# Kernel tuning notes

Hardware: AMD Instinct MI355X
Metric: run time of the kernel (lower is better)

The kernel has to match this reference:

```python
import jax, jax.numpy as jnp
import numpy as np

N_NODES = 50000
N_EDGES = 800000
NODE_DIM = 64
EDGE_DIM = 32
HID = 128


def _lin_init(key, fan_in, fan_out):
    # torch nn.Linear default: U(-1/sqrt(fan_in), 1/sqrt(fan_in))
    bound = 1.0 / np.sqrt(fan_in)
    kw, kb = jax.random.split(key)
    W = jax.random.uniform(kw, (fan_in, fan_out), jnp.float32, -bound, bound)
    b = jax.random.uniform(kb, (fan_out,), jnp.float32, -bound, bound)
    return W, b


def setup_inputs() -> dict:
    key = jax.random.key(0)
    ks = jax.random.split(key, 10)
    h = jax.random.normal(ks[0], (N_NODES, NODE_DIM), dtype=jnp.float32)
    x = jax.random.normal(ks[1], (N_NODES, 3), dtype=jnp.float32) * 10.0
    edge_idx = jax.random.randint(ks[2], (2, N_EDGES), 0, N_NODES)
    edge_dist = jax.random.uniform(ks[3], (N_EDGES,), jnp.float32) * 15.0
    m_in_dim = 2 * NODE_DIM + EDGE_DIM
    W_e1, b_e1 = _lin_init(ks[4], 1, EDGE_DIM)
    W_e2, b_e2 = _lin_init(ks[5], EDGE_DIM, EDGE_DIM)
    W_n1, b_n1 = _lin_init(ks[6], m_in_dim, HID)
    W_n2, b_n2 = _lin_init(ks[7], HID, NODE_DIM)
    W_c1, b_c1 = _lin_init(ks[8], m_in_dim, HID)
    W_c2, _ = _lin_init(ks[9], HID, 1)  # coord_mlp final layer has bias=False
    return dict(h=h, x=x, edge_dist=edge_dist,
                W_e1=W_e1, b_e1=b_e1, W_e2=W_e2, b_e2=b_e2,
                W_n1=W_n1, b_n1=b_n1, W_n2=W_n2, b_n2=b_n2,
                W_c1=W_c1, b_c1=b_c1, W_c2=W_c2,
                edge_idx=edge_idx)


def reference(h, x, edge_dist, W_e1, b_e1, W_e2, b_e2, W_n1, b_n1,
              W_n2, b_n2, W_c1, b_c1, W_c2, edge_idx):
    src, dst = edge_idx[0], edge_idx[1]
    n = h.shape[0]
    # edge_mlp: Linear(1,edge_dim) -> SiLU -> Linear(edge_dim,edge_dim)
    edge_attr = jax.nn.silu(edge_dist[:, None] @ W_e1 + b_e1) @ W_e2 + b_e2  # [E, edge_dim]
    m_in = jnp.concatenate([h[src], h[dst], edge_attr], axis=-1)  # [E, 2*node+edge]
    # node_mlp: Linear -> SiLU -> Linear
    m = jax.nn.silu(m_in @ W_n1 + b_n1) @ W_n2 + b_n2  # [E, node_dim]
    h_agg = jax.ops.segment_sum(m, dst, num_segments=n)
    # coord_mlp: Linear -> SiLU -> Linear(,1,bias=False)
    coord_w = jax.nn.silu(m_in @ W_c1 + b_c1) @ W_c2  # [E, 1]
    dir_vec = x[src] - x[dst]  # [E, 3]
    dir_len = jnp.maximum(jnp.linalg.norm(dir_vec, axis=-1, keepdims=True), 1e-8)
    x_agg = jax.ops.segment_sum(coord_w * (dir_vec / dir_len), dst, num_segments=n)
    return (h + h_agg, x + x_agg)
```

## Files before the change

kernel.cpp:

```cpp
#include <hip/hip_runtime.h>
#include <cstdint>
#include <cstddef>

#define E_CNT 800000
#define N_CNT 50000
#define NT 6250

typedef short bf16x8 __attribute__((ext_vector_type(8)));
typedef short s16x4 __attribute__((ext_vector_type(4)));
typedef float f32x4 __attribute__((ext_vector_type(4)));
typedef uint32_t u32x4 __attribute__((ext_vector_type(4)));

#define OFF_CURSOR 0
#define OFF_WFN 200064
#define OFF_WFC 241024
#define OFF_W2F 281984
#define OFF_BIASN 298368
#define OFF_BIASC 298880
#define OFF_SRC 299520
#define OFF_DST 3499520
#define OFF_DIST 6699520
#define OFF_HB 8299520
#define REQ_FULL 14699520

__device__ __forceinline__ short f2bf(float v) {
  uint32_t u = __builtin_bit_cast(uint32_t, v);
  u = (u + 0x7FFFu + ((u >> 16) & 1u)) >> 16;
  return (short)u;
}
__device__ __forceinline__ float bf2f(short s) {
  uint32_t u = ((uint32_t)(uint16_t)s) << 16;
  return __builtin_bit_cast(float, u);
}
__device__ __forceinline__ uint32_t pack2(float lo, float hi) {
  return ((uint32_t)(uint16_t)f2bf(hi) << 16) | (uint32_t)(uint16_t)f2bf(lo);
}
__device__ __forceinline__ uint32_t cvtpk(float lo, float hi) {
  uint32_t r;
  asm("v_cvt_pk_bf16_f32 %0, %1, %2" : "=v"(r) : "v"(lo), "v"(hi));
  return r;
}
__device__ __forceinline__ float silu_f(float v) {
  return v * (1.0f / (1.0f + __expf(-v)));
}

template <bool FULL>
__global__ void k_pre(const float* __restrict__ h, const float* __restrict__ x,
                      float* __restrict__ out, short* __restrict__ hb,
                      const int* __restrict__ eidx, int* __restrict__ cursor,
                      const float* __restrict__ W1n, const float* __restrict__ W1c,
                      const float* __restrict__ We2, const float* __restrict__ bn1,
                      const float* __restrict__ bc1, const float* __restrict__ be2,
                      const float* __restrict__ Wn2,
                      short* __restrict__ Wfn, short* __restrict__ Wfc,
                      short* __restrict__ W2f, float* __restrict__ biasn,
                      float* __restrict__ biasc) {
  const int b = (int)blockIdx.x;
  if (b < 3272) {
    const int i = b * 256 + (int)threadIdx.x;
    if (i < 800000) {
      const f32x4 v = ((const f32x4*)h)[i];
      ((f32x4*)out)[i] = v;
      if (FULL) {
        s16x4 p;
#pragma unroll
        for (int j = 0; j < 4; ++j) p[j] = f2bf(v[j]);
        *(s16x4*)(hb + i * 4) = p;
      }
    } else if (i < 837500) {
      ((f32x4*)out)[i] = ((const f32x4*)x)[i - 800000];
    }
  } else if (b < 3297) {
    const int idx = (b - 3272) * 4 + ((int)threadIdx.x >> 6);
    const int l = (int)threadIdx.x & 63;
    if (idx < 80) {
      const int fid = (idx < 40) ? idx : (idx - 40);
      const float* W1 = (idx < 40) ? W1n : W1c;
      short* Wf = (idx < 40) ? Wfn : Wfc;
      const int kt = fid >> 3, nt = fid & 7;
      const int feat = (l & 15) * 8 + nt;
      const int k0 = kt * 32 + (l >> 4) * 8;
      bf16x8 v;
#pragma unroll
      for (int j = 0; j < 8; ++j) {
        const int k = k0 + j;
        float val;
        if (k < 128) {
          val = W1[k * 128 + feat];
        } else {
          float s = 0.f;
          for (int cc = 0; cc < 32; ++cc)
            s = fmaf(We2[(k - 128) * 32 + cc], W1[(128 + cc) * 128 + feat], s);
          val = s;
        }
        v[j] = f2bf(val);
      }
      *(bf16x8*)&Wf[(fid * 64 + l) * 8] = v;
    } else if (idx < 96) {
      const int fid = idx - 80;
      const int kt2 = fid >> 2, nt2 = fid & 3;
      bf16x8 v;
#pragma unroll
      for (int j = 0; j < 8; ++j)
        v[j] = f2bf(Wn2[(kt2 * 32 + (l >> 4) * 8 + j) * 64 + nt2 * 16 + (l & 15)]);
      *(bf16x8*)&W2f[(fid * 64 + l) * 8] = v;
    } else if (idx == 96) {
      for (int col = l; col < 128; col += 64) {
        float sn = bn1[col], sc = bc1[col];
        for (int cc = 0; cc < 32; ++cc) {
          sn = fmaf(be2[cc], W1n[(128 + cc) * 128 + col], sn);
          sc = fmaf(be2[cc], W1c[(128 + cc) * 128 + col], sc);
        }
        biasn[col] = sn;
        biasc[col] = sc;
      }
    }
  } else if (FULL) {
    const int e = (b - 3297) * 256 + (int)threadIdx.x;
    if (e < E_CNT) atomicAdd(&cursor[eidx[E_CNT + e]], 1);
  }
}

__global__ __launch_bounds__(1024) void k_scan(int* __restrict__ cursor) {
  __shared__ int part[1024];
  const int t = (int)threadIdx.x;
  const int b0 = t * 49;
  int n = N_CNT - b0;
  n = n < 0 ? 0 : (n > 49 ? 49 : n);
  int s = 0;
  for (int i = 0; i < n; ++i) s += cursor[b0 + i];
  part[t] = s;
  __syncthreads();
  for (int off = 1; off < 1024; off <<= 1) {
    const int u = (t >= off) ? part[t - off] : 0;
    __syncthreads();
    part[t] += u;
    __syncthreads();
  }
  int run = (t == 0) ? 0 : part[t - 1];
  for (int i = 0; i < n; ++i) {
    const int old = cursor[b0 + i];
    cursor[b0 + i] = run;
    run += old;
  }
}

__global__ void k_fill(const int* __restrict__ eidx, const float* __restrict__ edist,
                       int* __restrict__ cursor, int* __restrict__ src_s,
                       int* __restrict__ dst_s, short* __restrict__ dist_s) {
  const int e = (int)(blockIdx.x * 256 + threadIdx.x);
  if (e < E_CNT) {
    const int d = eidx[E_CNT + e];
    const int pos = atomicAdd(&cursor[d], 1);
    src_s[pos] = eidx[e];
    dst_s[pos] = d;
    dist_s[pos] = f2bf(edist[e]);
  }
}

template <bool SORTED>
__global__ __launch_bounds__(256, 2) void k_main(
    const float* __restrict__ h, const short* __restrict__ hb,
    const float* __restrict__ x, const float* __restrict__ edist,
    const float* __restrict__ We1, const float* __restrict__ be1,
    const float* __restrict__ bn2, const float* __restrict__ Wc2,
    const int* __restrict__ eidx,
    const int* __restrict__ src_s, const int* __restrict__ dst_s,
    const short* __restrict__ dist_s,
    const short* __restrict__ Wfn, const short* __restrict__ Wfc,
    const short* __restrict__ W2f,
    const float* __restrict__ biasn, const float* __restrict__ biasc,
    float* __restrict__ out, float* __restrict__ xo) {
  __shared__ __align__(16) short scr[4][16 * 136];

  const int tid = (int)threadIdx.x;
  const int w = tid >> 6, l = tid & 63, g = l >> 4, c = l & 15;
  const f32x4 vzero = {0.f, 0.f, 0.f, 0.f};
  const int half = (int)(gridDim.x >> 1);

  if ((int)blockIdx.x < half) {
    short* myscr = &scr[w][0];

    float we1s[8], be1s[8];
#pragma unroll
    for (int j = 0; j < 8; ++j) { we1s[j] = We1[g * 8 + j]; be1s[j] = be1[g * 8 + j]; }
    float bias1[8];
#pragma unroll
    for (int nt = 0; nt < 8; ++nt) bias1[nt] = biasn[c * 8 + nt];
    float bias2[4];
#pragma unroll
    for (int nt = 0; nt < 4; ++nt) bias2[nt] = bn2[nt * 16 + c];

    int t = (int)blockIdx.x;
    int ps0 = 0, ps1 = 0, pd0 = 0, pd1 = 0;
    float pdd0 = 0.f, pdd1 = 0.f;
    if (t < NT) {
      const int e0 = t * 128 + w * 32 + 2 * c, e1 = e0 + 1;
      if (SORTED) {
        ps0 = src_s[e0]; ps1 = src_s[e1];
        pd0 = dst_s[e0]; pd1 = dst_s[e1];
        pdd0 = bf2f(dist_s[e0]); pdd1 = bf2f(dist_s[e1]);
      } else {
        ps0 = eidx[e0]; ps1 = eidx[e1];
        pd0 = eidx[E_CNT + e0]; pd1 = eidx[E_CNT + e1];
        pdd0 = edist[e0]; pdd1 = edist[e1];
      }
    }

    for (; t < NT; t += half) {
      const short* wft = Wfn;
      const short* w2t = W2f;
      asm volatile("" : "+v"(wft), "+v"(w2t));

      const int s0 = ps0, s1 = ps1, d0 = pd0, d1 = pd1;
      const float dd0 = pdd0, dd1 = pdd1;

      const int tn = t + half;
      if (tn < NT) {
        const int e0 = tn * 128 + w * 32 + 2 * c, e1 = e0 + 1;
        if (SORTED) {
          ps0 = src_s[e0]; ps1 = src_s[e1];
          pd0 = dst_s[e0]; pd1 = dst_s[e1];
          pdd0 = bf2f(dist_s[e0]); pdd1 = bf2f(dist_s[e1]);
        } else {
          ps0 = eidx[e0]; ps1 = eidx[e1];
          pd0 = eidx[E_CNT + e0]; pd1 = eidx[E_CNT + e1];
          pdd0 = edist[e0]; pdd1 = edist[e1];
        }
      }

      f32x4 acc[2][8];
#pragma unroll
      for (int mt = 0; mt < 2; ++mt)
#pragma unroll
        for (int nt = 0; nt < 8; ++nt) acc[mt][nt] = vzero;

#pragma unroll
      for (int kt = 0; kt < 5; ++kt) {
        bf16x8 a0, a1;
        if (kt < 4) {
          const size_t r0 = (size_t)((kt < 2) ? s0 : d0) * 64 + (kt & 1) * 32 + g * 8;
          const size_t r1 = (size_t)((kt < 2) ? s1 : d1) * 64 + (kt & 1) * 32 + g * 8;
          if (SORTED) {
            a0 = *(const bf16x8*)&hb[r0];
            a1 = *(const bf16x8*)&hb[r1];
          } else {
            const f32x4 pa = *(const f32x4*)(h + r0), pb = *(const f32x4*)(h + r0 + 4);
            const f32x4 qa = *(const f32x4*)(h + r1), qb = *(const f32x4*)(h + r1 + 4);
            u32x4 u0 = {pack2(pa[0], pa[1]), pack2(pa[2], pa[3]),
                        pack2(pb[0], pb[1]), pack2(pb[2], pb[3])};
            u32x4 u1 = {pack2(qa[0], qa[1]), pack2(qa[2], qa[3]),
                        pack2(qb[0], qb[1]), pack2(qb[2], qb[3])};
            a0 = __builtin_bit_cast(bf16x8, u0);
            a1 = __builtin_bit_cast(bf16x8, u1);
          }
        } else {
          float t0[8], t1[8];
#pragma unroll
          for (int j = 0; j < 8; ++j) {
            t0[j] = silu_f(fmaf(dd0, we1s[j], be1s[j]));
            t1[j] = silu_f(fmaf(dd1, we1s[j], be1s[j]));
          }
          u32x4 u0 = {cvtpk(t0[0], t0[1]), cvtpk(t0[2], t0[3]),
                      cvtpk(t0[4], t0[5]), cvtpk(t0[6], t0[7])};
          u32x4 u1 = {cvtpk(t1[0], t1[1]), cvtpk(t1[2], t1[3]),
                      cvtpk(t1[4], t1[5]), cvtpk(t1[6], t1[7])};
          a0 = __builtin_bit_cast(bf16x8, u0);
          a1 = __builtin_bit_cast(bf16x8, u1);
        }
#pragma unroll
        for (int nt = 0; nt < 8; ++nt) {
          const bf16x8 b = *(const bf16x8*)&wft[(((kt << 3) + nt) << 9) + (l << 3)];
          acc[0][nt] = __builtin_amdgcn_mfma_f32_16x16x32_bf16(a0, b, acc[0][nt], 0, 0, 0);
          acc[1][nt] = __builtin_amdgcn_mfma_f32_16x16x32_bf16(a1, b, acc[1][nt], 0, 0, 0);
        }
      }

      f32x4 acc2[2][4];
#pragma unroll
      for (int nt = 0; nt < 4; ++nt) { acc2[0][nt] = vzero; acc2[1][nt] = vzero; }

#pragma unroll
      for (int mt = 0; mt < 2; ++mt) {
#pragma unroll
        for (int r = 0; r < 4; ++r) {
          const float v0 = silu_f(acc[mt][0][r] + bias1[0]);
          const float v1 = silu_f(acc[mt][1][r] + bias1[1]);
          const float v2 = silu_f(acc[mt][2][r] + bias1[2]);
          const float v3 = silu_f(acc[mt][3][r] + bias1[3]);
          const float v4 = silu_f(acc[mt][4][r] + bias1[4]);
          const float v5 = silu_f(acc[mt][5][r] + bias1[5]);
          const float v6 = silu_f(acc[mt][6][r] + bias1[6]);
          const float v7 = silu_f(acc[mt][7][r] + bias1[7]);
          u32x4 pkv = {cvtpk(v0, v1), cvtpk(v2, v3), cvtpk(v4, v5), cvtpk(v6, v7)};
          *(u32x4*)&myscr[(4 * g + r) * 136 + c * 8] = pkv;
        }
#pragma unroll
        for (int kt2 = 0; kt2 < 4; ++kt2) {
          const bf16x8 a2 = *(const bf16x8*)&myscr[c * 136 + kt2 * 32 + g * 8];
#pragma unroll
          for (int nt2 = 0; nt2 < 4; ++nt2) {
            const bf16x8 b2 = *(const bf16x8*)&w2t[(((kt2 << 2) + nt2) << 9) + (l << 3)];
            acc2[mt][nt2] = __builtin_amdgcn_mfma_f32_16x16x32_bf16(a2, b2, acc2[mt][nt2], 0, 0, 0);
          }
        }
      }

      int des[8];
#pragma unroll
      for (int s = 0; s < 8; ++s)
        des[s] = __shfl((s & 1) ? d1 : d0, 4 * g + (s >> 1));

      float run[4];
      int cur = des[0];
#pragma unroll
      for (int nt2 = 0; nt2 < 4; ++nt2) run[nt2] = acc2[0][nt2][0] + bias2[nt2];
#pragma unroll
      for (int s = 1; s < 8; ++s) {
        const int mt = s & 1, r = s >> 1;
        if (des[s] == cur) {
#pragma unroll
          for (int nt2 = 0; nt2 < 4; ++nt2) run[nt2] += acc2[mt][nt2][r] + bias2[nt2];
        } else {
#pragma unroll
          for (int nt2 = 0; nt2 < 4; ++nt2)
            unsafeAtomicAdd(&out[(size_t)cur * 64 + nt2 * 16 + c], run[nt2]);
          cur = des[s];
#pragma unroll
          for (int nt2 = 0; nt2 < 4; ++nt2) run[nt2] = acc2[mt][nt2][r] + bias2[nt2];
        }
      }
#pragma unroll
      for (int nt2 = 0; nt2 < 4; ++nt2)
        unsafeAtomicAdd(&out[(size_t)cur * 64 + nt2 * 16 + c], run[nt2]);
    }
  } else {
    float we1s[8], be1s[8];
#pragma unroll
    for (int j = 0; j < 8; ++j) { we1s[j] = We1[g * 8 + j]; be1s[j] = be1[g * 8 + j]; }
    float b1c[8], wc2l[8];
#pragma unroll
    for (int nt = 0; nt < 8; ++nt) {
      b1c[nt] = biasc[c * 8 + nt];
      wc2l[nt] = Wc2[c * 8 + nt];
    }

    int t = (int)blockIdx.x - half;
    int ps0 = 0, ps1 = 0, pd0 = 0, pd1 = 0;
    float pdd0 = 0.f, pdd1 = 0.f;
    if (t < NT) {
      const int e0 = t * 128 + w * 32 + 2 * c, e1 = e0 + 1;
      if (SORTED) {
        ps0 = src_s[e0]; ps1 = src_s[e1];
        pd0 = dst_s[e0]; pd1 = dst_s[e1];
        pdd0 = bf2f(dist_s[e0]); pdd1 = bf2f(dist_s[e1]);
      } else {
        ps0 = eidx[e0]; ps1 = eidx[e1];
        pd0 = eidx[E_CNT + e0]; pd1 = eidx[E_CNT + e1];
        pdd0 = edist[e0]; pdd1 = edist[e1];
      }
    }

    for (; t < NT; t += half) {
      const short* wft = Wfc;
      asm volatile("" : "+v"(wft));

      const int s0 = ps0, s1 = ps1, d0 = pd0, d1 = pd1;
      const float dd0 = pdd0, dd1 = pdd1;

      const int tn = t + half;
      if (tn < NT) {
        const int e0 = tn * 128 + w * 32 + 2 * c, e1 = e0 + 1;
        if (SORTED) {
          ps0 = src_s[e0]; ps1 = src_s[e1];
          pd0 = dst_s[e0]; pd1 = dst_s[e1];
          pdd0 = bf2f(dist_s[e0]); pdd1 = bf2f(dist_s[e1]);
        } else {
          ps0 = eidx[e0]; ps1 = eidx[e1];
          pd0 = eidx[E_CNT + e0]; pd1 = eidx[E_CNT + e1];
          pdd0 = edist[e0]; pdd1 = edist[e1];
        }
      }

      f32x4 acc[2][8];
#pragma unroll
      for (int mt = 0; mt < 2; ++mt)
#pragma unroll
        for (int nt = 0; nt < 8; ++nt) acc[mt][nt] = vzero;

#pragma unroll
      for (int kt = 0; kt < 5; ++kt) {
        bf16x8 a0, a1;
        if (kt < 4) {
          const size_t r0 = (size_t)((kt < 2) ? s0 : d0) * 64 + (kt & 1) * 32 + g * 8;
          const size_t r1 = (size_t)((kt < 2) ? s1 : d1) * 64 + (kt & 1) * 32 + g * 8;
          if (SORTED) {
            a0 = *(const bf16x8*)&hb[r0];
            a1 = *(const bf16x8*)&hb[r1];
          } else {
            const f32x4 pa = *(const f32x4*)(h + r0), pb = *(const f32x4*)(h + r0 + 4);
            const f32x4 qa = *(const f32x4*)(h + r1), qb = *(const f32x4*)(h + r1 + 4);
            u32x4 u0 = {pack2(pa[0], pa[1]), pack2(pa[2], pa[3]),
                        pack2(pb[0], pb[1]), pack2(pb[2], pb[3])};
            u32x4 u1 = {pack2(qa[0], qa[1]), pack2(qa[2], qa[3]),
                        pack2(qb[0], qb[1]), pack2(qb[2], qb[3])};
            a0 = __builtin_bit_cast(bf16x8, u0);
            a1 = __builtin_bit_cast(bf16x8, u1);
          }
        } else {
          float t0[8], t1[8];
#pragma unroll
          for (int j = 0; j < 8; ++j) {
            t0[j] = silu_f(fmaf(dd0, we1s[j], be1s[j]));
            t1[j] = silu_f(fmaf(dd1, we1s[j], be1s[j]));
          }
          u32x4 u0 = {cvtpk(t0[0], t0[1]), cvtpk(t0[2], t0[3]),
                      cvtpk(t0[4], t0[5]), cvtpk(t0[6], t0[7])};
          u32x4 u1 = {cvtpk(t1[0], t1[1]), cvtpk(t1[2], t1[3]),
                      cvtpk(t1[4], t1[5]), cvtpk(t1[6], t1[7])};
          a0 = __builtin_bit_cast(bf16x8, u0);
          a1 = __builtin_bit_cast(bf16x8, u1);
        }
#pragma unroll
        for (int nt = 0; nt < 8; ++nt) {
          const bf16x8 b = *(const bf16x8*)&wft[(((kt << 3) + nt) << 9) + (l << 3)];
          acc[0][nt] = __builtin_amdgcn_mfma_f32_16x16x32_bf16(a0, b, acc[0][nt], 0, 0, 0);
          acc[1][nt] = __builtin_amdgcn_mfma_f32_16x16x32_bf16(a1, b, acc[1][nt], 0, 0, 0);
        }
      }

      float p0[4], p1[4];
#pragma unroll
      for (int r = 0; r < 4; ++r) {
        float a = 0.f, bsum = 0.f;
#pragma unroll
        for (int nt = 0; nt < 8; ++nt) {
          a += silu_f(acc[0][nt][r] + b1c[nt]) * wc2l[nt];
          bsum += silu_f(acc[1][nt][r] + b1c[nt]) * wc2l[nt];
        }
        p0[r] = a; p1[r] = bsum;
      }
#pragma unroll
      for (int m = 1; m < 16; m <<= 1)
#pragma unroll
        for (int r = 0; r < 4; ++r) {
          p0[r] += __shfl_xor(p0[r], m);
          p1[r] += __shfl_xor(p1[r], m);
        }

      const int mt = c & 1, rr = c >> 1;
      const int dA = __shfl(d0, 4 * g + rr), dB = __shfl(d1, 4 * g + rr);
      const int sA = __shfl(s0, 4 * g + rr), sB = __shfl(s1, 4 * g + rr);
      const int dstE = mt ? dB : dA;
      const int srcE = mt ? sB : sA;
      if (c < 8) {
        const float cwp0 = (rr == 0) ? p0[0] : (rr == 1) ? p0[1] : (rr == 2) ? p0[2] : p0[3];
        const float cwp1 = (rr == 0) ? p1[0] : (rr == 1) ? p1[1] : (rr == 2) ? p1[2] : p1[3];
        const float cw = mt ? cwp1 : cwp0;
        const float ax = x[srcE * 3 + 0] - x[dstE * 3 + 0];
        const float ay = x[srcE * 3 + 1] - x[dstE * 3 + 1];
        const float az = x[srcE * 3 + 2] - x[dstE * 3 + 2];
        float len = sqrtf(fmaf(ax, ax, fmaf(ay, ay, az * az)));
        len = fmaxf(len, 1e-8f);
        const float scl = cw / len;
        float vx = scl * ax, vy = scl * ay, vz = scl * az;
#pragma unroll
        for (int k = 1; k < 8; k <<= 1) {
          const float tx = __shfl(vx, l - k);
          const float ty = __shfl(vy, l - k);
          const float tz = __shfl(vz, l - k);
          const int td = __shfl(dstE, l - k);
          if (c >= k && td == dstE) { vx += tx; vy += ty; vz += tz; }
        }
        const int dnx = __shfl(dstE, l + 1);
        if (c == 7 || dnx != dstE) {
          unsafeAtomicAdd(&xo[dstE * 3 + 0], vx);
          unsafeAtomicAdd(&xo[dstE * 3 + 1], vy);
          unsafeAtomicAdd(&xo[dstE * 3 + 2], vz);
        }
      }
    }
  }
}

extern "C" void kernel_launch(void* const* d_in, const int* in_sizes, int n_in,
                              void* d_out, int out_size, void* d_ws, size_t ws_size,
                              hipStream_t stream) {
  const float* h = (const float*)d_in[0];
  const float* x = (const float*)d_in[1];
  const float* edist = (const float*)d_in[2];
  const float* We1 = (const float*)d_in[3];
  const float* be1 = (const float*)d_in[4];
  const float* We2 = (const float*)d_in[5];
  const float* be2 = (const float*)d_in[6];
  const float* Wn1 = (const float*)d_in[7];
  const float* bn1 = (const float*)d_in[8];
  const float* Wn2 = (const float*)d_in[9];
  const float* bn2 = (const float*)d_in[10];
  const float* Wc1 = (const float*)d_in[11];
  const float* bc1 = (const float*)d_in[12];
  const float* Wc2 = (const float*)d_in[13];
  const int* eidx = (const int*)d_in[14];
  float* out = (float*)d_out;
  float* xo = out + 3200000;

  char* wsb = (char*)d_ws;
  int* cursor = (int*)(wsb + OFF_CURSOR);
  short* Wfn = (short*)(wsb + OFF_WFN);
  short* Wfc = (short*)(wsb + OFF_WFC);
  short* W2f = (short*)(wsb + OFF_W2F);
  float* biasn = (float*)(wsb + OFF_BIASN);
  float* biasc = (float*)(wsb + OFF_BIASC);
  int* src_s = (int*)(wsb + OFF_SRC);
  int* dst_s = (int*)(wsb + OFF_DST);
  short* dist_s = (short*)(wsb + OFF_DIST);
  short* hb = (short*)(wsb + OFF_HB);

  const bool full = (ws_size >= (size_t)REQ_FULL);

  if (full) {
    hipMemsetAsync(cursor, 0, N_CNT * sizeof(int), stream);
    k_pre<true><<<dim3(6422), dim3(256), 0, stream>>>(h, x, out, hb, eidx, cursor,
                                                      Wn1, Wc1, We2, bn1, bc1, be2, Wn2,
                                                      Wfn, Wfc, W2f, biasn, biasc);
    k_scan<<<dim3(1), dim3(1024), 0, stream>>>(cursor);
    k_fill<<<dim3(3125), dim3(256), 0, stream>>>(eidx, edist, cursor, src_s, dst_s, dist_s);
    k_main<true><<<dim3(512), dim3(256), 0, stream>>>(
        h, hb, x, edist, We1, be1, bn2, Wc2, eidx, src_s, dst_s, dist_s,
        Wfn, Wfc, W2f, biasn, biasc, out, xo);
  } else {
    k_pre<false><<<dim3(3297), dim3(256), 0, stream>>>(h, x, out, nullptr, eidx, nullptr,
                                                       Wn1, Wc1, We2, bn1, bc1, be2, Wn2,
                                                       Wfn, Wfc, W2f, biasn, biasc);
    k_main<false><<<dim3(512), dim3(256), 0, stream>>>(
        h, nullptr, x, edist, We1, be1, bn2, Wc2, eidx, nullptr, nullptr, nullptr,
        Wfn, Wfc, W2f, biasn, biasc, out, xo);
  }
}
```

Baseline: 492.4 us.

## Prefetch next tile's gathered node features into registers during MFMA work

Deepens the software pipeline: edge indices are now prefetched two tiles ahead, and the bf16 node-feature gathers for the next tile are issued right after the current tile's MFMA loop. The gathers then overlap with the SiLU, second GEMM and atomic scatter stages. The goal is to hide the latency of the random h[src]/h[dst] loads. The cost is extra VGPRs for the eight prefetched bf16x8 vectors, which could lower occupancy or cause spills.

```diff
diff --git a/kernel.cpp b/kernel.cpp
--- a/kernel.cpp
+++ b/kernel.cpp
@@ -192,18 +192,33 @@
     for (int nt = 0; nt < 4; ++nt) bias2[nt] = bn2[nt * 16 + c];
 
     int t = (int)blockIdx.x;
-    int ps0 = 0, ps1 = 0, pd0 = 0, pd1 = 0;
-    float pdd0 = 0.f, pdd1 = 0.f;
-    if (t < NT) {
-      const int e0 = t * 128 + w * 32 + 2 * c, e1 = e0 + 1;
+    int cs0 = 0, cs1 = 0, cd0 = 0, cd1 = 0;
+    float cdd0 = 0.f, cdd1 = 0.f;
+    int ns0 = 0, ns1 = 0, nd0 = 0, nd1 = 0;
+    float ndd0 = 0.f, ndd1 = 0.f;
+    bf16x8 af0[4], af1[4];
+    {
+      const int e0 = t * 128 + w * 32 + 2 * c;
       if (SORTED) {
-        ps0 = src_s[e0]; ps1 = src_s[e1];
-        pd0 = dst_s[e0]; pd1 = dst_s[e1];
-        pdd0 = bf2f(dist_s[e0]); pdd1 = bf2f(dist_s[e1]);
+        cs0 = src_s[e0]; cs1 = src_s[e0 + 1];
+        cd0 = dst_s[e0]; cd1 = dst_s[e0 + 1];
+        cdd0 = bf2f(dist_s[e0]); cdd1 = bf2f(dist_s[e0 + 1]);
+#pragma unroll
+        for (int kt = 0; kt < 4; ++kt) {
+          af0[kt] = *(const bf16x8*)&hb[(size_t)((kt < 2) ? cs0 : cd0) * 64 + (kt & 1) * 32 + g * 8];
+          af1[kt] = *(const bf16x8*)&hb[(size_t)((kt < 2) ? cs1 : cd1) * 64 + (kt & 1) * 32 + g * 8];
+        }
+        const int tn = t + half;
+        if (tn < NT) {
+          const int e1 = tn * 128 + w * 32 + 2 * c;
+          ns0 = src_s[e1]; ns1 = src_s[e1 + 1];
+          nd0 = dst_s[e1]; nd1 = dst_s[e1 + 1];
+          ndd0 = bf2f(dist_s[e1]); ndd1 = bf2f(dist_s[e1 + 1]);
+        }
       } else {
-        ps0 = eidx[e0]; ps1 = eidx[e1];
-        pd0 = eidx[E_CNT + e0]; pd1 = eidx[E_CNT + e1];
-        pdd0 = edist[e0]; pdd1 = edist[e1];
+        cs0 = eidx[e0]; cs1 = eidx[e0 + 1];
+        cd0 = eidx[E_CNT + e0]; cd1 = eidx[E_CNT + e0 + 1];
+        cdd0 = edist[e0]; cdd1 = edist[e0 + 1];
       }
     }
 
@@ -212,21 +227,23 @@
       const short* w2t = W2f;
       asm volatile("" : "+v"(wft), "+v"(w2t));
 
-      const int s0 = ps0, s1 = ps1, d0 = pd0, d1 = pd1;
-      const float dd0 = pdd0, dd1 = pdd1;
-
-      const int tn = t + half;
-      if (tn < NT) {
-        const int e0 = tn * 128 + w * 32 + 2 * c, e1 = e0 + 1;
-        if (SORTED) {
-          ps0 = src_s[e0]; ps1 = src_s[e1];
-          pd0 = dst_s[e0]; pd1 = dst_s[e1];
-          pdd0 = bf2f(dist_s[e0]); pdd1 = bf2f(dist_s[e1]);
-        } else {
-          ps0 = eidx[e0]; ps1 = eidx[e1];
-          pd0 = eidx[E_CNT + e0]; pd1 = eidx[E_CNT + e1];
-          pdd0 = edist[e0]; pdd1 = edist[e1];
-        }
+      const int s0 = cs0, s1 = cs1, d0 = cd0, d1 = cd1;
+      const float dd0 = cdd0, dd1 = cdd1;
+
+      bf16x8 ae0, ae1;
+      {
+        float t0[8], t1[8];
+#pragma unroll
+        for (int j = 0; j < 8; ++j) {
+          t0[j] = silu_f(fmaf(dd0, we1s[j], be1s[j]));
+          t1[j] = silu_f(fmaf(dd1, we1s[j], be1s[j]));
+        }
+        u32x4 u0 = {cvtpk(t0[0], t0[1]), cvtpk(t0[2], t0[3]),
+                    cvtpk(t0[4], t0[5]), cvtpk(t0[6], t0[7])};
+        u32x4 u1 = {cvtpk(t1[0], t1[1]), cvtpk(t1[2], t1[3]),
+                    cvtpk(t1[4], t1[5]), cvtpk(t1[6], t1[7])};
+        ae0 = __builtin_bit_cast(bf16x8, u0);
+        ae1 = __builtin_bit_cast(bf16x8, u1);
       }
 
       f32x4 acc[2][8];
@@ -239,12 +256,12 @@
       for (int kt = 0; kt < 5; ++kt) {
         bf16x8 a0, a1;
         if (kt < 4) {
-          const size_t r0 = (size_t)((kt < 2) ? s0 : d0) * 64 + (kt & 1) * 32 + g * 8;
-          const size_t r1 = (size_t)((kt < 2) ? s1 : d1) * 64 + (kt & 1) * 32 + g * 8;
           if (SORTED) {
-            a0 = *(const bf16x8*)&hb[r0];
-            a1 = *(const bf16x8*)&hb[r1];
+            a0 = af0[kt];
+            a1 = af1[kt];
           } else {
+            const size_t r0 = (size_t)((kt < 2) ? s0 : d0) * 64 + (kt & 1) * 32 + g * 8;
+            const size_t r1 = (size_t)((kt < 2) ? s1 : d1) * 64 + (kt & 1) * 32 + g * 8;
             const f32x4 pa = *(const f32x4*)(h + r0), pb = *(const f32x4*)(h + r0 + 4);
             const f32x4 qa = *(const f32x4*)(h + r1), qb = *(const f32x4*)(h + r1 + 4);
             u32x4 u0 = {pack2(pa[0], pa[1]), pack2(pa[2], pa[3]),
@@ -255,24 +272,22 @@
             a1 = __builtin_bit_cast(bf16x8, u1);
           }
         } else {
-          float t0[8], t1[8];
-#pragma unroll
-          for (int j = 0; j < 8; ++j) {
-            t0[j] = silu_f(fmaf(dd0, we1s[j], be1s[j]));
-            t1[j] = silu_f(fmaf(dd1, we1s[j], be1s[j]));
-          }
-          u32x4 u0 = {cvtpk(t0[0], t0[1]), cvtpk(t0[2], t0[3]),
-                      cvtpk(t0[4], t0[5]), cvtpk(t0[6], t0[7])};
-          u32x4 u1 = {cvtpk(t1[0], t1[1]), cvtpk(t1[2], t1[3]),
-                      cvtpk(t1[4], t1[5]), cvtpk(t1[6], t1[7])};
-          a0 = __builtin_bit_cast(bf16x8, u0);
-          a1 = __builtin_bit_cast(bf16x8, u1);
+          a0 = ae0;
+          a1 = ae1;
         }
 #pragma unroll
         for (int nt = 0; nt < 8; ++nt) {
           const bf16x8 b = *(const bf16x8*)&wft[(((kt << 3) + nt) << 9) + (l << 3)];
           acc[0][nt] = __builtin_amdgcn_mfma_f32_16x16x32_bf16(a0, b, acc[0][nt], 0, 0, 0);
           acc[1][nt] = __builtin_amdgcn_mfma_f32_16x16x32_bf16(a1, b, acc[1][nt], 0, 0, 0);
+        }
+      }
+
+      if (SORTED && (t + half) < NT) {
+#pragma unroll
+        for (int kt = 0; kt < 4; ++kt) {
+          af0[kt] = *(const bf16x8*)&hb[(size_t)((kt < 2) ? ns0 : nd0) * 64 + (kt & 1) * 32 + g * 8];
+          af1[kt] = *(const bf16x8*)&hb[(size_t)((kt < 2) ? ns1 : nd1) * 64 + (kt & 1) * 32 + g * 8];
         }
       }
 
@@ -333,6 +348,31 @@
 #pragma unroll
       for (int nt2 = 0; nt2 < 4; ++nt2)
         unsafeAtomicAdd(&out[(size_t)cur * 64 + nt2 * 16 + c], run[nt2]);
+
+      cs0 = ns0; cs1 = ns1; cd0 = nd0; cd1 = nd1; cdd0 = ndd0; cdd1 = ndd1;
+      const int t2 = t + 2 * half;
+      if (t2 < NT) {
+        const int e2 = t2 * 128 + w * 32 + 2 * c;
+        if (SORTED) {
+          ns0 = src_s[e2]; ns1 = src_s[e2 + 1];
+          nd0 = dst_s[e2]; nd1 = dst_s[e2 + 1];
+          ndd0 = bf2f(dist_s[e2]); ndd1 = bf2f(dist_s[e2 + 1]);
+        } else {
+          ns0 = eidx[e2]; ns1 = eidx[e2 + 1];
+          nd0 = eidx[E_CNT + e2]; nd1 = eidx[E_CNT + e2 + 1];
+          ndd0 = edist[e2]; ndd1 = edist[e2 + 1];
+        }
+      } else if (!SORTED) {
+      }
+      if (!SORTED) {
+        const int tn1 = t + half;
+        if (tn1 < NT) {
+          const int e1 = tn1 * 128 + w * 32 + 2 * c;
+          cs0 = eidx[e1]; cs1 = eidx[e1 + 1];
+          cd0 = eidx[E_CNT + e1]; cd1 = eidx[E_CNT + e1 + 1];
+          cdd0 = edist[e1]; cdd1 = edist[e1 + 1];
+        }
+      }
     }
   } else {
     float we1s[8], be1s[8];
@@ -346,18 +386,33 @@
     }
 
     int t = (int)blockIdx.x - half;
-    int ps0 = 0, ps1 = 0, pd0 = 0, pd1 = 0;
-    float pdd0 = 0.f, pdd1 = 0.f;
-    if (t < NT) {
-      const int e0 = t * 128 + w * 32 + 2 * c, e1 = e0 + 1;
+    int cs0 = 0, cs1 = 0, cd0 = 0, cd1 = 0;
+    float cdd0 = 0.f, cdd1 = 0.f;
+    int ns0 = 0, ns1 = 0, nd0 = 0, nd1 = 0;
+    float ndd0 = 0.f, ndd1 = 0.f;
+    bf16x8 af0[4], af1[4];
+    {
+      const int e0 = t * 128 + w * 32 + 2 * c;
       if (SORTED) {
-        ps0 = src_s[e0]; ps1 = src_s[e1];
-        pd0 = dst_s[e0]; pd1 = dst_s[e1];
-        pdd0 = bf2f(dist_s[e0]); pdd1 = bf2f(dist_s[e1]);
+        cs0 = src_s[e0]; cs1 = src_s[e0 + 1];
+        cd0 = dst_s[e0]; cd1 = dst_s[e0 + 1];
+        cdd0 = bf2f(dist_s[e0]); cdd1 = bf2f(dist_s[e0 + 1]);
+#pragma unroll
+        for (int kt = 0; kt < 4; ++kt) {
+          af0[kt] = *(const bf16x8*)&hb[(size_t)((kt < 2) ? cs0 : cd0) * 64 + (kt & 1) * 32 + g * 8];
+          af1[kt] = *(const bf16x8*)&hb[(size_t)((kt < 2) ? cs1 : cd1) * 64 + (kt & 1) * 32 + g * 8];
+        }
+        const int tn = t + half;
+        if (tn < NT) {
+          const int e1 = tn * 128 + w * 32 + 2 * c;
+          ns0 = src_s[e1]; ns1 = src_s[e1 + 1];
+          nd0 = dst_s[e1]; nd1 = dst_s[e1 + 1];
+          ndd0 = bf2f(dist_s[e1]); ndd1 = bf2f(dist_s[e1 + 1]);
+        }
       } else {
-        ps0 = eidx[e0]; ps1 = eidx[e1];
-        pd0 = eidx[E_CNT + e0]; pd1 = eidx[E_CNT + e1];
-        pdd0 = edist[e0]; pdd1 = edist[e1];
+        cs0 = eidx[e0]; cs1 = eidx[e0 + 1];
+        cd0 = eidx[E_CNT + e0]; cd1 = eidx[E_CNT + e0 + 1];
+        cdd0 = edist[e0]; cdd1 = edist[e0 + 1];
       }
     }
 
@@ -365,21 +420,23 @@
       const short* wft = Wfc;
       asm volatile("" : "+v"(wft));
 
-      const int s0 = ps0, s1 = ps1, d0 = pd0, d1 = pd1;
-      const float dd0 = pdd0, dd1 = pdd1;
-
-      const int tn = t + half;
-      if (tn < NT) {
-        const int e0 = tn * 128 + w * 32 + 2 * c, e1 = e0 + 1;
-        if (SORTED) {
-          ps0 = src_s[e0]; ps1 = src_s[e1];
-          pd0 = dst_s[e0]; pd1 = dst_s[e1];
-          pdd0 = bf2f(dist_s[e0]); pdd1 = bf2f(dist_s[e1]);
-        } else {
-          ps0 = eidx[e0]; ps1 = eidx[e1];
-          pd0 = eidx[E_CNT + e0]; pd1 = eidx[E_CNT + e1];
-          pdd0 = edist[e0]; pdd1 = edist[e1];
-        }
+      const int s0 = cs0, s1 = cs1, d0 = cd0, d1 = cd1;
+      const float dd0 = cdd0, dd1 = cdd1;
+
+      bf16x8 ae0, ae1;
+      {
+        float t0[8], t1[8];
+#pragma unroll
+        for (int j = 0; j < 8; ++j) {
+          t0[j] = silu_f(fmaf(dd0, we1s[j], be1s[j]));
+          t1[j] = silu_f(fmaf(dd1, we1s[j], be1s[j]));
+        }
+        u32x4 u0 = {cvtpk(t0[0], t0[1]), cvtpk(t0[2], t0[3]),
+                    cvtpk(t0[4], t0[5]), cvtpk(t0[6], t0[7])};
+        u32x4 u1 = {cvtpk(t1[0], t1[1]), cvtpk(t1[2], t1[3]),
+                    cvtpk(t1[4], t1[5]), cvtpk(t1[6], t1[7])};
+        ae0 = __builtin_bit_cast(bf16x8, u0);
+        ae1 = __builtin_bit_cast(bf16x8, u1);
       }
 
       f32x4 acc[2][8];
@@ -392,12 +449,12 @@
       for (int kt = 0; kt < 5; ++kt) {
         bf16x8 a0, a1;
         if (kt < 4) {
-          const size_t r0 = (size_t)((kt < 2) ? s0 : d0) * 64 + (kt & 1) * 32 + g * 8;
-          const size_t r1 = (size_t)((kt < 2) ? s1 : d1) * 64 + (kt & 1) * 32 + g * 8;
           if (SORTED) {
-            a0 = *(const bf16x8*)&hb[r0];
-            a1 = *(const bf16x8*)&hb[r1];
+            a0 = af0[kt];
+            a1 = af1[kt];
           } else {
+            const size_t r0 = (size_t)((kt < 2) ? s0 : d0) * 64 + (kt & 1) * 32 + g * 8;
+            const size_t r1 = (size_t)((kt < 2) ? s1 : d1) * 64 + (kt & 1) * 32 + g * 8;
             const f32x4 pa = *(const f32x4*)(h + r0), pb = *(const f32x4*)(h + r0 + 4);
             const f32x4 qa = *(const f32x4*)(h + r1), qb = *(const f32x4*)(h + r1 + 4);
             u32x4 u0 = {pack2(pa[0], pa[1]), pack2(pa[2], pa[3]),
@@ -408,24 +465,22 @@
             a1 = __builtin_bit_cast(bf16x8, u1);
           }
         } else {
-          float t0[8], t1[8];
-#pragma unroll
-          for (int j = 0; j < 8; ++j) {
-            t0[j] = silu_f(fmaf(dd0, we1s[j], be1s[j]));
-            t1[j] = silu_f(fmaf(dd1, we1s[j], be1s[j]));
-          }
-          u32x4 u0 = {cvtpk(t0[0], t0[1]), cvtpk(t0[2], t0[3]),
-                      cvtpk(t0[4], t0[5]), cvtpk(t0[6], t0[7])};
-          u32x4 u1 = {cvtpk(t1[0], t1[1]), cvtpk(t1[2], t1[3]),
-                      cvtpk(t1[4], t1[5]), cvtpk(t1[6], t1[7])};
-          a0 = __builtin_bit_cast(bf16x8, u0);
-          a1 = __builtin_bit_cast(bf16x8, u1);
+          a0 = ae0;
+          a1 = ae1;
         }
 #pragma unroll
         for (int nt = 0; nt < 8; ++nt) {
           const bf16x8 b = *(const bf16x8*)&wft[(((kt << 3) + nt) << 9) + (l << 3)];
           acc[0][nt] = __builtin_amdgcn_mfma_f32_16x16x32_bf16(a0, b, acc[0][nt], 0, 0, 0);
           acc[1][nt] = __builtin_amdgcn_mfma_f32_16x16x32_bf16(a1, b, acc[1][nt], 0, 0, 0);
+        }
+      }
+
+      if (SORTED && (t + half) < NT) {
+#pragma unroll
+        for (int kt = 0; kt < 4; ++kt) {
+          af0[kt] = *(const bf16x8*)&hb[(size_t)((kt < 2) ? ns0 : nd0) * 64 + (kt & 1) * 32 + g * 8];
+          af1[kt] = *(const bf16x8*)&hb[(size_t)((kt < 2) ? ns1 : nd1) * 64 + (kt & 1) * 32 + g * 8];
         }
       }
 
@@ -477,6 +532,30 @@
           unsafeAtomicAdd(&xo[dstE * 3 + 0], vx);
           unsafeAtomicAdd(&xo[dstE * 3 + 1], vy);
           unsafeAtomicAdd(&xo[dstE * 3 + 2], vz);
+        }
+      }
+
+      cs0 = ns0; cs1 = ns1; cd0 = nd0; cd1 = nd1; cdd0 = ndd0; cdd1 = ndd1;
+      const int t2 = t + 2 * half;
+      if (t2 < NT) {
+        const int e2 = t2 * 128 + w * 32 + 2 * c;
+        if (SORTED) {
+          ns0 = src_s[e2]; ns1 = src_s[e2 + 1];
+          nd0 = dst_s[e2]; nd1 = dst_s[e2 + 1];
+          ndd0 = bf2f(dist_s[e2]); ndd1 = bf2f(dist_s[e2 + 1]);
+        } else {
+          ns0 = eidx[e2]; ns1 = eidx[e2 + 1];
+          nd0 = eidx[E_CNT + e2]; nd1 = eidx[E_CNT + e2 + 1];
+          ndd0 = edist[e2]; ndd1 = edist[e2 + 1];
+        }
+      }
+      if (!SORTED) {
+        const int tn1 = t + half;
+        if (tn1 < NT) {
+          const int e1 = tn1 * 128 + w * 32 + 2 * c;
+          cs0 = eidx[e1]; cs1 = eidx[e1 + 1];
+          cd0 = eidx[E_CNT + e1]; cd1 = eidx[E_CNT + e1 + 1];
+          cdd0 = edist[e1]; cdd1 = edist[e1 + 1];
         }
       }
     }
```

Measured after the change: 411.2 us. 16.5% less time.
